# Kernel optimization log

Hardware: AMD Instinct MI355X
Metric: run time of the kernel (lower is better)

Reference implementation:

```python
import jax, jax.numpy as jnp
import numpy as np

B, IDF, RES = 32, 64, 128
CDF, SRC_L, A_DIM = 768, 18, 100
QUERY_L = RES * RES


def setup_inputs() -> dict:
    key = jax.random.key(0)
    ks = jax.random.split(key, 5)
    inputs = jax.random.normal(ks[0], (B, IDF, RES, RES), dtype=jnp.float32)
    context = jax.random.normal(ks[1], (B, CDF, SRC_L), dtype=jnp.float32)
    conv_ctx_w = jax.random.normal(ks[2], (IDF, CDF), dtype=jnp.float32) * (1.0 / np.sqrt(CDF))
    conv_w = jax.random.normal(ks[3], (IDF,), dtype=jnp.float32) * (1.0 / np.sqrt(IDF))
    conv_b = jnp.zeros((1,), dtype=jnp.float32)
    fc_w = jax.random.normal(ks[4], (A_DIM, QUERY_L), dtype=jnp.float32) * (1.0 / np.sqrt(QUERY_L))
    fc_b = jnp.zeros((A_DIM,), dtype=jnp.float32)
    return {"inputs": inputs, "context": context, "conv_ctx_w": conv_ctx_w,
            "conv_w": conv_w, "conv_b": conv_b, "fc_w": fc_w, "fc_b": fc_b}


def reference(inputs, context, conv_ctx_w, conv_w, conv_b, fc_w, fc_b):
    b, idf, ih, iw = inputs.shape
    queryL = ih * iw
    # target: [b, idf, queryL]
    target = inputs.reshape(b, idf, queryL)
    # 1x1 conv on context (conv_context): [b, idf, sourceL]
    sourceT = jnp.einsum('ic,bcs->bis', conv_ctx_w, context)
    # attn scores: [b, queryL, sourceL]; softmax over sourceL (dim=1 on flattened view)
    attn = jnp.einsum('biq,bis->bqs', target, sourceT)
    attn = jax.nn.softmax(attn, axis=-1)
    # weighted context: [b, idf, queryL]
    wctx = jnp.einsum('bis,bqs->biq', sourceT, attn)
    # 1x1 conv to single channel (self.conv): [b, queryL]
    wctx = jnp.einsum('i,biq->bq', conv_w, wctx) + conv_b
    # att_fc: [b, a_dim]
    out = wctx @ fc_w.T + fc_b
    return out
```

## Files before the change

### kernel.cpp

```cpp
#include <hip/hip_runtime.h>

#define BB 32
#define IDF 64
#define QL 16384
#define CDF 768
#define SL 18
#define SLP 20
#define ADIM 100

__device__ __forceinline__ void fma4(float4& a, const float4 v, const float s) {
    a.x += v.x * s; a.y += v.y * s; a.z += v.z * s; a.w += v.w * s;
}

__global__ __launch_bounds__(256, 2) void kA_source(
        const float* __restrict__ ctx,
        const float* __restrict__ wic,
        const float* __restrict__ fc_b,
        float* __restrict__ sT,
        float* __restrict__ out)
{
    __shared__ __align__(16) float ctx_l[CDF * SLP];
    const int b = blockIdx.x;
    const int g = blockIdx.y;

    if (g == 0) {
        const int t = b * 256 + threadIdx.x;
        if (t < BB * ADIM) out[t] = fc_b[t % ADIM];
    }

    const float* ctxb = ctx + (size_t)b * CDF * SL;
    for (int t = threadIdx.x; t < CDF * SL; t += 256) {
        const int c = t / SL;
        const int s = t - c * SL;
        ctx_l[c * SLP + s] = ctxb[t];
    }
    __syncthreads();

    const int wave = threadIdx.x >> 6;
    const int lane = threadIdx.x & 63;
    const int i0 = g * 16 + wave * 4;

    float acc[4][SL];
#pragma unroll
    for (int ii = 0; ii < 4; ii++)
#pragma unroll
        for (int s = 0; s < SL; s++) acc[ii][s] = 0.f;

    for (int k = 0; k < CDF / 64; k++) {
        const int c = k * 64 + lane;
        float wv[4];
#pragma unroll
        for (int ii = 0; ii < 4; ii++) wv[ii] = wic[(i0 + ii) * CDF + c];
        float r[SLP];
        const float4* r4 = (const float4*)&ctx_l[c * SLP];
        ((float4*)r)[0] = r4[0];
        ((float4*)r)[1] = r4[1];
        ((float4*)r)[2] = r4[2];
        ((float4*)r)[3] = r4[3];
        ((float4*)r)[4] = r4[4];
#pragma unroll
        for (int ii = 0; ii < 4; ii++)
#pragma unroll
            for (int s = 0; s < SL; s++) acc[ii][s] += wv[ii] * r[s];
    }

#pragma unroll
    for (int ii = 0; ii < 4; ii++) {
#pragma unroll
        for (int s = 0; s < SL; s++) {
            float a = acc[ii][s];
#pragma unroll
            for (int off = 32; off; off >>= 1) a += __shfl_xor(a, off, 64);
            if (lane == 0) sT[((size_t)b * IDF + i0 + ii) * SLP + s] = a;
        }
    }
}

__global__ __launch_bounds__(256, 2) void kB_attn_fc(
        const float* __restrict__ inp,
        const float* __restrict__ sT,
        const float* __restrict__ conv_w,
        const float* __restrict__ conv_b,
        const float* __restrict__ fcw,
        float* __restrict__ out)
{
    __shared__ __align__(16) float st_l[IDF * SLP];
    __shared__ __align__(16) float wq_l[1024];
    __shared__ float cw_l[IDF];
    __shared__ float v_l[SL];
    const int b  = blockIdx.y;
    const int qt = blockIdx.x;
    const int tid = threadIdx.x;
    const int wave = tid >> 6;
    const int lane = tid & 63;

    for (int t = tid; t < IDF * SLP; t += 256) st_l[t] = sT[(size_t)b * IDF * SLP + t];
    if (tid < IDF) cw_l[tid] = conv_w[tid];
    __syncthreads();
    if (tid < SL) {
        float a = 0.f;
#pragma unroll
        for (int i = 0; i < IDF; i++) a += cw_l[i] * st_l[i * SLP + tid];
        v_l[tid] = a;
    }
    __syncthreads();

    const int q = (qt * 256 + tid) * 4;
    const float4* ip4 = (const float4*)(inp + (size_t)b * IDF * QL + q);

    float4 sc[SL];
#pragma unroll
    for (int s = 0; s < SL; s++) sc[s] = make_float4(0.f, 0.f, 0.f, 0.f);

#pragma unroll 8
    for (int i = 0; i < IDF; i++) {
        const float4 x = ip4[(size_t)i * (QL / 4)];
        float r[SLP];
        const float4* r4 = (const float4*)&st_l[i * SLP];
        ((float4*)r)[0] = r4[0];
        ((float4*)r)[1] = r4[1];
        ((float4*)r)[2] = r4[2];
        ((float4*)r)[3] = r4[3];
        ((float4*)r)[4] = r4[4];
#pragma unroll
        for (int s = 0; s < SL; s++) fma4(sc[s], x, r[s]);
    }

    float4 m = sc[0];
#pragma unroll
    for (int s = 1; s < SL; s++) {
        m.x = fmaxf(m.x, sc[s].x); m.y = fmaxf(m.y, sc[s].y);
        m.z = fmaxf(m.z, sc[s].z); m.w = fmaxf(m.w, sc[s].w);
    }
    float4 l = make_float4(0.f, 0.f, 0.f, 0.f);
    float4 o = make_float4(0.f, 0.f, 0.f, 0.f);
#pragma unroll
    for (int s = 0; s < SL; s++) {
        const float vs = v_l[s];
        float4 p;
        p.x = __expf(sc[s].x - m.x); p.y = __expf(sc[s].y - m.y);
        p.z = __expf(sc[s].z - m.z); p.w = __expf(sc[s].w - m.w);
        l.x += p.x; l.y += p.y; l.z += p.z; l.w += p.w;
        o.x += p.x * vs; o.y += p.y * vs; o.z += p.z * vs; o.w += p.w * vs;
    }
    const float cb = conv_b[0];
    float4 res;
    res.x = o.x / l.x + cb; res.y = o.y / l.y + cb;
    res.z = o.z / l.z + cb; res.w = o.w / l.w + cb;
    ((float4*)wq_l)[tid] = res;
    __syncthreads();

    const float* fcw_t = fcw + (size_t)qt * 1024;
#pragma unroll 1
    for (int aa = 0; aa < 25; aa++) {
        const int a = wave * 25 + aa;
        const float* fr = fcw_t + (size_t)a * QL;
        float acc = 0.f;
#pragma unroll
        for (int pass = 0; pass < 4; pass++) {
            const int qi = pass * 256 + lane * 4;
            const float4 f = *(const float4*)(fr + qi);
            const float4 w = *(const float4*)(wq_l + qi);
            acc += f.x * w.x + f.y * w.y + f.z * w.z + f.w * w.w;
        }
#pragma unroll
        for (int off = 32; off; off >>= 1) acc += __shfl_xor(acc, off, 64);
        if (lane == 0) atomicAdd(&out[b * ADIM + a], acc);
    }
}

extern "C" void kernel_launch(void* const* d_in, const int* in_sizes, int n_in,
                              void* d_out, int out_size, void* d_ws, size_t ws_size,
                              hipStream_t stream)
{
    const float* inputs     = (const float*)d_in[0];
    const float* context    = (const float*)d_in[1];
    const float* conv_ctx_w = (const float*)d_in[2];
    const float* conv_w     = (const float*)d_in[3];
    const float* conv_b     = (const float*)d_in[4];
    const float* fc_w       = (const float*)d_in[5];
    const float* fc_b       = (const float*)d_in[6];
    float* out = (float*)d_out;

    float* ws = (float*)d_ws;
    float* sT = ws;

    kA_source<<<dim3(BB, 4), dim3(256), 0, stream>>>(context, conv_ctx_w, fc_b, sT, out);
    kB_attn_fc<<<dim3(16, BB), dim3(256), 0, stream>>>(inputs, sT, conv_w, conv_b, fc_w, out);
}
```

Before: 271.7 us.

## Double grid parallelism with float2 per thread and register prefetch of inputs

```diff
diff --git a/kernel.cpp b/kernel.cpp
--- a/kernel.cpp
+++ b/kernel.cpp
@@ -8,10 +8,6 @@
 #define SLP 20
 #define ADIM 100
 
-__device__ __forceinline__ void fma4(float4& a, const float4 v, const float s) {
-    a.x += v.x * s; a.y += v.y * s; a.z += v.z * s; a.w += v.w * s;
-}
-
 __global__ __launch_bounds__(256, 2) void kA_source(
         const float* __restrict__ ctx,
         const float* __restrict__ wic,
@@ -19,60 +15,42 @@
         float* __restrict__ sT,
         float* __restrict__ out)
 {
-    __shared__ __align__(16) float ctx_l[CDF * SLP];
-    const int b = blockIdx.x;
-    const int g = blockIdx.y;
+    const int blk  = blockIdx.x;
+    const int tid  = threadIdx.x;
+    const int wave = tid >> 6;
+    const int lane = tid & 63;
 
-    if (g == 0) {
-        const int t = b * 256 + threadIdx.x;
+    if (blk < 13) {
+        const int t = blk * 256 + tid;
         if (t < BB * ADIM) out[t] = fc_b[t % ADIM];
     }
 
+    const int b = blk >> 4;
+    const int i = (blk & 15) * 4 + wave;
     const float* ctxb = ctx + (size_t)b * CDF * SL;
-    for (int t = threadIdx.x; t < CDF * SL; t += 256) {
-        const int c = t / SL;
-        const int s = t - c * SL;
-        ctx_l[c * SLP + s] = ctxb[t];
-    }
-    __syncthreads();
+    const float* wrow = wic + (size_t)i * CDF;
 
-    const int wave = threadIdx.x >> 6;
-    const int lane = threadIdx.x & 63;
-    const int i0 = g * 16 + wave * 4;
+    float acc[SL];
+#pragma unroll
+    for (int s = 0; s < SL; s++) acc[s] = 0.f;
 
-    float acc[4][SL];
-#pragma unroll
-    for (int ii = 0; ii < 4; ii++)
-#pragma unroll
-        for (int s = 0; s < SL; s++) acc[ii][s] = 0.f;
-
+#pragma unroll 2
     for (int k = 0; k < CDF / 64; k++) {
         const int c = k * 64 + lane;
-        float wv[4];
+        const float wv = wrow[c];
+        const float* cr = ctxb + (size_t)c * SL;
+        float r[SL];
 #pragma unroll
-        for (int ii = 0; ii < 4; ii++) wv[ii] = wic[(i0 + ii) * CDF + c];
-        float r[SLP];
-        const float4* r4 = (const float4*)&ctx_l[c * SLP];
-        ((float4*)r)[0] = r4[0];
-        ((float4*)r)[1] = r4[1];
-        ((float4*)r)[2] = r4[2];
-        ((float4*)r)[3] = r4[3];
-        ((float4*)r)[4] = r4[4];
+        for (int s = 0; s < SL; s++) r[s] = cr[s];
 #pragma unroll
-        for (int ii = 0; ii < 4; ii++)
+        for (int s = 0; s < SL; s++) acc[s] += wv * r[s];
+    }
 #pragma unroll
-            for (int s = 0; s < SL; s++) acc[ii][s] += wv[ii] * r[s];
-    }
-
+    for (int s = 0; s < SL; s++) {
+        float a = acc[s];
 #pragma unroll
-    for (int ii = 0; ii < 4; ii++) {
-#pragma unroll
-        for (int s = 0; s < SL; s++) {
-            float a = acc[ii][s];
-#pragma unroll
-            for (int off = 32; off; off >>= 1) a += __shfl_xor(a, off, 64);
-            if (lane == 0) sT[((size_t)b * IDF + i0 + ii) * SLP + s] = a;
-        }
+        for (int off = 32; off; off >>= 1) a += __shfl_xor(a, off, 64);
+        if (lane == 0) sT[((size_t)b * IDF + i) * SLP + s] = a;
     }
 }
 
@@ -85,11 +63,11 @@
         float* __restrict__ out)
 {
     __shared__ __align__(16) float st_l[IDF * SLP];
-    __shared__ __align__(16) float wq_l[1024];
+    __shared__ __align__(16) float wq_l[512];
     __shared__ float cw_l[IDF];
     __shared__ float v_l[SL];
-    const int b  = blockIdx.y;
-    const int qt = blockIdx.x;
+    const int b   = blockIdx.y;
+    const int qt  = blockIdx.x;
     const int tid = threadIdx.x;
     const int wave = tid >> 6;
     const int lane = tid & 63;
@@ -105,64 +83,71 @@
     }
     __syncthreads();
 
-    const int q = (qt * 256 + tid) * 4;
-    const float4* ip4 = (const float4*)(inp + (size_t)b * IDF * QL + q);
+    const float2* ip2 = (const float2*)(inp + (size_t)b * IDF * QL + (size_t)qt * 512);
 
-    float4 sc[SL];
+    float2 sc[SL];
 #pragma unroll
-    for (int s = 0; s < SL; s++) sc[s] = make_float4(0.f, 0.f, 0.f, 0.f);
+    for (int s = 0; s < SL; s++) sc[s] = make_float2(0.f, 0.f);
 
-#pragma unroll 8
+    float2 xb[4];
+#pragma unroll
+    for (int j = 0; j < 4; j++) xb[j] = ip2[(size_t)j * (QL / 2) + tid];
+
+#pragma unroll 4
     for (int i = 0; i < IDF; i++) {
-        const float4 x = ip4[(size_t)i * (QL / 4)];
-        float r[SLP];
+        const float2 x = xb[i & 3];
+        if (i + 4 < IDF) xb[i & 3] = ip2[(size_t)(i + 4) * (QL / 2) + tid];
+        float r[SL];
         const float4* r4 = (const float4*)&st_l[i * SLP];
         ((float4*)r)[0] = r4[0];
         ((float4*)r)[1] = r4[1];
         ((float4*)r)[2] = r4[2];
         ((float4*)r)[3] = r4[3];
-        ((float4*)r)[4] = r4[4];
+        ((float2*)(r + 16))[0] = *(const float2*)&st_l[i * SLP + 16];
 #pragma unroll
-        for (int s = 0; s < SL; s++) fma4(sc[s], x, r[s]);
+        for (int s = 0; s < SL; s++) {
+            sc[s].x += x.x * r[s];
+            sc[s].y += x.y * r[s];
+        }
     }
 
-    float4 m = sc[0];
+    float2 m = sc[0];
 #pragma unroll
     for (int s = 1; s < SL; s++) {
-        m.x = fmaxf(m.x, sc[s].x); m.y = fmaxf(m.y, sc[s].y);
-        m.z = fmaxf(m.z, sc[s].z); m.w = fmaxf(m.w, sc[s].w);
+        m.x = fmaxf(m.x, sc[s].x);
+        m.y = fmaxf(m.y, sc[s].y);
     }
-    float4 l = make_float4(0.f, 0.f, 0.f, 0.f);
-    float4 o = make_float4(0.f, 0.f, 0.f, 0.f);
+    float2 l = make_float2(0.f, 0.f);
+    float2 o = make_float2(0.f, 0.f);
 #pragma unroll
     for (int s = 0; s < SL; s++) {
         const float vs = v_l[s];
-        float4 p;
-        p.x = __expf(sc[s].x - m.x); p.y = __expf(sc[s].y - m.y);
-        p.z = __expf(sc[s].z - m.z); p.w = __expf(sc[s].w - m.w);
-        l.x += p.x; l.y += p.y; l.z += p.z; l.w += p.w;
-        o.x += p.x * vs; o.y += p.y * vs; o.z += p.z * vs; o.w += p.w * vs;
+        float2 p;
+        p.x = __expf(sc[s].x - m.x);
+        p.y = __expf(sc[s].y - m.y);
+        l.x += p.x; l.y += p.y;
+        o.x += p.x * vs; o.y += p.y * vs;
     }
     const float cb = conv_b[0];
-    float4 res;
-    res.x = o.x / l.x + cb; res.y = o.y / l.y + cb;
-    res.z = o.z / l.z + cb; res.w = o.w / l.w + cb;
-    ((float4*)wq_l)[tid] = res;
+    float2 res;
+    res.x = o.x / l.x + cb;
+    res.y = o.y / l.y + cb;
+    ((float2*)wq_l)[tid] = res;
     __syncthreads();
 
-    const float* fcw_t = fcw + (size_t)qt * 1024;
+    float wv[8];
+    ((float4*)wv)[0] = *(const float4*)&wq_l[lane * 8];
+    ((float4*)wv)[1] = *(const float4*)&wq_l[lane * 8 + 4];
+
+    const float* fcw_t = fcw + (size_t)qt * 512;
 #pragma unroll 1
     for (int aa = 0; aa < 25; aa++) {
         const int a = wave * 25 + aa;
-        const float* fr = fcw_t + (size_t)a * QL;
-        float acc = 0.f;
-#pragma unroll
-        for (int pass = 0; pass < 4; pass++) {
-            const int qi = pass * 256 + lane * 4;
-            const float4 f = *(const float4*)(fr + qi);
-            const float4 w = *(const float4*)(wq_l + qi);
-            acc += f.x * w.x + f.y * w.y + f.z * w.z + f.w * w.w;
-        }
+        const float* fr = fcw_t + (size_t)a * QL + lane * 8;
+        float4 f0 = *(const float4*)fr;
+        float4 f1 = *(const float4*)(fr + 4);
+        float acc = f0.x * wv[0] + f0.y * wv[1] + f0.z * wv[2] + f0.w * wv[3]
+                  + f1.x * wv[4] + f1.y * wv[5] + f1.z * wv[6] + f1.w * wv[7];
 #pragma unroll
         for (int off = 32; off; off >>= 1) acc += __shfl_xor(acc, off, 64);
         if (lane == 0) atomicAdd(&out[b * ADIM + a], acc);
@@ -185,6 +170,6 @@
     float* ws = (float*)d_ws;
     float* sT = ws;
 
-    kA_source<<<dim3(BB, 4), dim3(256), 0, stream>>>(context, conv_ctx_w, fc_b, sT, out);
-    kB_attn_fc<<<dim3(16, BB), dim3(256), 0, stream>>>(inputs, sT, conv_w, conv_b, fc_w, out);
+    kA_source<<<dim3(512), dim3(256), 0, stream>>>(context, conv_ctx_w, fc_b, sT, out);
+    kB_attn_fc<<<dim3(32, BB), dim3(256), 0, stream>>>(inputs, sT, conv_w, conv_b, fc_w, out);
 }
```

Measured after the change: 239.7 us. -11.8%, faster.
